# Kernel tuning notes

Hardware: AMD Instinct MI355X
Metric: run time of the kernel (lower is better)

## Reference

```python
import jax, jax.numpy as jnp
import numpy as np

C = 1.0          # Poincare ball curvature
EPS = 1e-7       # clamp epsilon used by the torch code


def _expmap0(u, c=C):
    # geoopt PoincareBall.expmap0: tanh(sqrt(c)||u||) * u / (sqrt(c)||u||)
    sc = jnp.sqrt(c)
    n = jnp.maximum(jnp.linalg.norm(u, axis=-1, keepdims=True), 1e-15)
    return jnp.tanh(sc * n) * u / (sc * n)


def _hyp_dist_sq(x, y, c=C):
    # Pairwise squared Poincare distance WITHOUT materializing [nq,nc,d]:
    # d(x,y) = (2/sqrt(c)) * artanh(sqrt(c) * ||mobius_add(-x, y)||)
    # ||mobius_add(-x,y)||^2 expands into dot products and squared norms.
    dot = x @ y.T                                  # [nq, nc]
    xn = jnp.sum(x * x, axis=-1)[:, None]          # [nq, 1]
    yn = jnp.sum(y * y, axis=-1)[None, :]          # [1, nc]
    alpha = 1.0 - 2.0 * c * dot + c * yn
    beta = 1.0 - c * xn
    num_sq = alpha * alpha * xn - 2.0 * alpha * beta * dot + beta * beta * yn
    den = jnp.maximum(1.0 - 2.0 * c * dot + c * c * xn * yn, 1e-15)
    t = jnp.sqrt(c) * jnp.sqrt(jnp.maximum(num_sq, 0.0)) / den
    t = jnp.clip(t, 0.0, 1.0 - EPS)
    d = (2.0 / jnp.sqrt(c)) * jnp.arctanh(t)
    return d * d


def _project(x, We, be, Wh, bh, Ws, bs, scale_h):
    e = x @ We.T + be
    e = e / jnp.linalg.norm(e, axis=-1, keepdims=True)
    h = _expmap0((x @ Wh.T + bh) * scale_h)
    s = x @ Ws.T + bs
    s = s / jnp.linalg.norm(s, axis=-1, keepdims=True)
    return e, h, s


def setup_inputs() -> dict:
    key = jax.random.key(0)
    ks = jax.random.split(key, 12)
    D, NQ, NC = 768, 512, 65536
    def lin(k, out_d, in_d):
        lim = 1.0 / np.sqrt(in_d)
        k1, k2 = jax.random.split(k)
        W = jax.random.uniform(k1, (out_d, in_d), jnp.float32, -lim, lim)
        b = jax.random.uniform(k2, (out_d,), jnp.float32, -lim, lim)
        return W, b
    We, be = lin(ks[0], 32, D)
    Wh, bh = lin(ks[1], 16, D)
    Ws, bs = lin(ks[2], 16, D)
    W1, b1 = lin(ks[3], 32, D)
    W2, b2 = lin(ks[4], 3, 32)
    return {
        'x_q': jax.random.normal(ks[5], (NQ, D), jnp.float32),
        'x_c': jax.random.normal(ks[6], (NC, D), jnp.float32),
        'We': We, 'be': be, 'Wh': Wh, 'bh': bh, 'Ws': Ws, 'bs': bs,
        'scale_h': jnp.float32(0.3),
        'W1': W1, 'b1': b1, 'W2': W2, 'b2': b2,
    }


def reference(x_q, x_c, We, be, Wh, bh, Ws, bs, scale_h, W1, b1, W2, b2):
    # forward() projections for queries and corpus
    q_e, q_h, q_s = _project(x_q, We, be, Wh, bh, Ws, bs, scale_h)
    c_e, c_h, c_s = _project(x_c, We, be, Wh, bh, Ws, bs, scale_h)
    # get_weights(): softplus MLP on raw query embedding -> [nq, 3]
    w = jax.nn.softplus(jax.nn.relu(x_q @ W1.T + b1) @ W2.T + b2)
    # batch_retrieve math, fully vectorized
    dist_e = 2.0 - 2.0 * (q_e @ c_e.T)                       # unit vecs: ||a-b||^2
    dots = jnp.clip(q_s @ c_s.T, -1.0 + EPS, 1.0 - EPS)
    dist_s = jnp.arccos(dots) ** 2
    dist_h = _hyp_dist_sq(q_h, c_h)
    total = w[:, 0:1] * dist_e + w[:, 1:2] * dist_h + w[:, 2:3] * dist_s
    return -total
```

## Files before the change

kernel.cpp:

```cpp
#include <hip/hip_runtime.h>
#include <math.h>

#define NQ 512
#define NC 65536
#define DIM 768
#define PC_ROWS 128

typedef unsigned short u16;
typedef float f32x4 __attribute__((ext_vector_type(4)));
typedef short bf16x8 __attribute__((ext_vector_type(8)));

#define MFMA16(A, B, C) __builtin_amdgcn_mfma_f32_16x16x32_bf16(A, B, C, 0, 0, 0)

__device__ __forceinline__ u16 f2bf(float x) {
  union { float f; unsigned int u; } v; v.f = x;
  unsigned int r = v.u + 0x7fffu + ((v.u >> 16) & 1u);
  return (u16)(r >> 16);
}
__device__ __forceinline__ float bf2f(u16 h) {
  union { unsigned int u; float f; } v; v.u = ((unsigned int)h) << 16;
  return v.f;
}
__device__ __forceinline__ unsigned int pk2(u16 a, u16 b) {
  return (unsigned int)a | ((unsigned int)b << 16);
}

__device__ __forceinline__ float acos_poly(float x) {
  float z = fabsf(x);
  float p = -0.0012624911f;
  p = fmaf(p, z, 0.0066700901f);
  p = fmaf(p, z, -0.0170881256f);
  p = fmaf(p, z, 0.0308918810f);
  p = fmaf(p, z, -0.0501743046f);
  p = fmaf(p, z, 0.0889789874f);
  p = fmaf(p, z, -0.2145988016f);
  p = fmaf(p, z, 1.5707963050f);
  float r = __builtin_amdgcn_sqrtf(1.0f - z) * p;
  return (x < 0.0f) ? (3.14159265358979f - r) : r;
}

__global__ __launch_bounds__(256) void build_wpak(
    const float* __restrict__ We, const float* __restrict__ Ws,
    const float* __restrict__ Wh, u16* __restrict__ wpak)
{
  int id = blockIdx.x * 256 + threadIdx.x;
  int j = id & 7;
  int lane = (id >> 3) & 63;
  int nt = (id >> 9) & 3;
  int kc = id >> 11;
  int o = nt * 16 + (lane & 15);
  int k = kc * 32 + ((lane >> 4) & 3) * 8 + j;
  const float* Wrow = (o < 32) ? We + (size_t)o * DIM
                    : (o < 48) ? Ws + (size_t)(o - 32) * DIM
                               : Wh + (size_t)(o - 48) * DIM;
  float w = Wrow[k];
  u16 hi = f2bf(w);
  u16 lo = f2bf(w - bf2f(hi));
  size_t base = (((size_t)kc * 4 + nt) * 2 * 64 + lane) * 8 + j;
  wpak[base] = hi;
  wpak[base + 512] = lo;
}

__global__ __launch_bounds__(128) void proj_q(
    const float* __restrict__ xq,
    const float* __restrict__ We, const float* __restrict__ be,
    const float* __restrict__ Wh, const float* __restrict__ bh,
    const float* __restrict__ Ws, const float* __restrict__ bs,
    const float* __restrict__ shp,
    const float* __restrict__ W1, const float* __restrict__ b1,
    const float* __restrict__ W2, const float* __restrict__ b2,
    u16* __restrict__ qpak, float* __restrict__ qmeta)
{
  __shared__ __align__(16) float xrow[DIM];
  __shared__ float vals[96];
  __shared__ float reluv[32];
  __shared__ float hv[16];
  __shared__ float stats[8];
  const int t = threadIdx.x;
  const int q = blockIdx.x;

  for (int i = t; i < DIM; i += 128) xrow[i] = xq[(size_t)q * DIM + i];
  __syncthreads();

  if (t < 96) {
    const float* wr;
    float bias;
    if (t < 32)      { wr = We + (size_t)t * DIM;        bias = be[t]; }
    else if (t < 48) { wr = Ws + (size_t)(t - 32) * DIM; bias = bs[t - 32]; }
    else if (t < 64) { wr = Wh + (size_t)(t - 48) * DIM; bias = bh[t - 48]; }
    else             { wr = W1 + (size_t)(t - 64) * DIM; bias = b1[t - 64]; }
    const float4* x4 = (const float4*)xrow;
    const float4* w4 = (const float4*)wr;
    float acc = 0.0f;
    #pragma unroll 4
    for (int k = 0; k < DIM / 4; ++k) {
      float4 a = x4[k];
      float4 b = w4[k];
      acc = fmaf(a.x, b.x, acc);
      acc = fmaf(a.y, b.y, acc);
      acc = fmaf(a.z, b.z, acc);
      acc = fmaf(a.w, b.w, acc);
    }
    acc += bias;
    if (t >= 48 && t < 64) acc *= shp[0];
    vals[t] = acc;
  }
  __syncthreads();
  if (t < 32) reluv[t] = fmaxf(vals[64 + t], 0.0f);
  __syncthreads();

  if (t == 0) {
    float s = 0.0f;
    for (int j = 0; j < 32; ++j) s += vals[j] * vals[j];
    stats[0] = sqrtf(s);
  } else if (t == 1) {
    float s = 0.0f;
    for (int j = 32; j < 48; ++j) s += vals[j] * vals[j];
    stats[1] = sqrtf(s);
  } else if (t == 2) {
    float s = 0.0f;
    for (int j = 48; j < 64; ++j) s += vals[j] * vals[j];
    float n = fmaxf(sqrtf(s), 1e-15f);
    float f = tanhf(n) / n;
    float xn = 0.0f;
    for (int j = 0; j < 16; ++j) {
      float hj = vals[48 + j] * f;
      hv[j] = hj;
      xn += hj * hj;
    }
    stats[2] = xn;
    stats[3] = 1.0f - xn;
  } else if (t >= 3 && t < 6) {
    int m = t - 3;
    float s = 0.0f;
    for (int j = 0; j < 32; ++j) s = fmaf(reluv[j], W2[m * 32 + j], s);
    s += b2[m];
    stats[4 + m] = fmaxf(s, 0.0f) + log1pf(expf(-fabsf(s)));
  }
  __syncthreads();

  u16* qp = qpak + (size_t)q * 192;
  if (t < 32) {
    float v = vals[t] / stats[0];
    u16 hi = f2bf(v);
    u16 lo = f2bf(v - bf2f(hi));
    qp[t] = hi; qp[32 + t] = lo;
  } else if (t < 48) {
    int j = t - 32;
    float v = vals[t] / stats[1];
    u16 hi = f2bf(v);
    u16 lo = f2bf(v - bf2f(hi));
    qp[64 + j] = hi;  qp[80 + j] = hi;
    qp[96 + j] = lo;  qp[112 + j] = lo;
  } else if (t < 64) {
    int j = t - 48;
    float v = hv[j];
    u16 hi = f2bf(v);
    u16 lo = f2bf(v - bf2f(hi));
    qp[128 + j] = hi; qp[144 + j] = hi;
    qp[160 + j] = lo; qp[176 + j] = lo;
  } else if (t == 64) qmeta[(size_t)q * 8 + 0] = stats[2];
  else if (t == 65)   qmeta[(size_t)q * 8 + 1] = stats[3];
  else if (t >= 66 && t < 69) qmeta[(size_t)q * 8 + (t - 66 + 2)] = stats[4 + (t - 66)];
}

__global__ __launch_bounds__(256) void proj_corpus(
    const float* __restrict__ xc, const u16* __restrict__ wpak,
    const float* __restrict__ be, const float* __restrict__ bh,
    const float* __restrict__ bs, const float* __restrict__ shp,
    u16* __restrict__ cpak, float* __restrict__ cyn)
{
  __shared__ float lds[8320];
  u16* xpk = (u16*)lds;
  float (*vals)[65] = (float(*)[65])lds;
  __shared__ float biasc[64];
  __shared__ float shv;

  const int tid = threadIdx.x;
  const int lane = tid & 63;
  const int wv = tid >> 6;
  const int lr = lane & 15;
  const int lg = lane >> 4;
  const int r0 = blockIdx.x * PC_ROWS;

  if (tid < 64) {
    biasc[tid] = (tid < 32) ? be[tid] : (tid < 48) ? bs[tid - 32] : bh[tid - 48];
    if (tid == 0) shv = shp[0];
  }

  f32x4 acc[2][4];
  #pragma unroll
  for (int rt = 0; rt < 2; ++rt)
    #pragma unroll
    for (int nt = 0; nt < 4; ++nt)
      acc[rt][nt] = (f32x4){0.0f, 0.0f, 0.0f, 0.0f};

  for (int kc = 0; kc < 24; ++kc) {
    __syncthreads();
    #pragma unroll
    for (int i = 0; i < 4; ++i) {
      int p = tid + 256 * i;
      int row = p >> 3;
      int kq = p & 7;
      const float4 v = *(const float4*)(xc + (size_t)(r0 + row) * DIM + kc * 32 + 4 * kq);
      u16 hx = f2bf(v.x), hy = f2bf(v.y), hz = f2bf(v.z), hw = f2bf(v.w);
      u16 lx = f2bf(v.x - bf2f(hx)), ly = f2bf(v.y - bf2f(hy));
      u16 lz = f2bf(v.z - bf2f(hz)), lw = f2bf(v.w - bf2f(hw));
      uint2 hvv = {pk2(hx, hy), pk2(hz, hw)};
      uint2 lvv = {pk2(lx, ly), pk2(lz, lw)};
      int rm = row & 7;
      int qh = (kq >> 1) ^ rm;
      int ql = (4 + (kq >> 1)) ^ rm;
      int half = (kq & 1) * 8;
      *(uint2*)((char*)xpk + row * 128 + qh * 16 + half) = hvv;
      *(uint2*)((char*)xpk + row * 128 + ql * 16 + half) = lvv;
    }
    __syncthreads();

    const u16* wb = wpak + (size_t)kc * 4096;
    bf16x8 Bh[4], Bl[4];
    #pragma unroll
    for (int nt = 0; nt < 4; ++nt) {
      Bh[nt] = *(const bf16x8*)(wb + (nt * 2 + 0) * 512 + lane * 8);
      Bl[nt] = *(const bf16x8*)(wb + (nt * 2 + 1) * 512 + lane * 8);
    }

    #pragma unroll
    for (int rt = 0; rt < 2; ++rt) {
      int rowi = wv * 32 + rt * 16 + lr;
      int rm = rowi & 7;
      bf16x8 Ah = *(const bf16x8*)((const char*)xpk + rowi * 128 + (lg ^ rm) * 16);
      bf16x8 Al = *(const bf16x8*)((const char*)xpk + rowi * 128 + ((4 + lg) ^ rm) * 16);
      #pragma unroll
      for (int nt = 0; nt < 4; ++nt) {
        acc[rt][nt] = MFMA16(Ah, Bh[nt], acc[rt][nt]);
        acc[rt][nt] = MFMA16(Al, Bh[nt], acc[rt][nt]);
        acc[rt][nt] = MFMA16(Ah, Bl[nt], acc[rt][nt]);
      }
    }
  }
  __syncthreads();

  #pragma unroll
  for (int rt = 0; rt < 2; ++rt)
    #pragma unroll
    for (int nt = 0; nt < 4; ++nt)
      #pragma unroll
      for (int reg = 0; reg < 4; ++reg) {
        int row = wv * 32 + rt * 16 + lg * 4 + reg;
        int o = nt * 16 + lr;
        float v = acc[rt][nt][reg] + biasc[o];
        if (o >= 48) v *= shv;
        vals[row][o] = v;
      }
  __syncthreads();

  const int part = tid >> 7;
  const int row = tid & 127;
  const size_t g = (size_t)(r0 + row);
  u16* cp = cpak + g * 128;
  if (part == 0) {
    float ssum = 0.0f;
    for (int j = 0; j < 32; ++j) ssum += vals[row][j] * vals[row][j];
    float inv = 1.0f / sqrtf(ssum);
    for (int j = 0; j < 32; ++j) {
      float v = vals[row][j] * inv;
      u16 hi = f2bf(v);
      cp[j] = hi;
      cp[32 + j] = f2bf(v - bf2f(hi));
    }
  } else {
    float ssum = 0.0f;
    for (int j = 32; j < 48; ++j) ssum += vals[row][j] * vals[row][j];
    float inv = 1.0f / sqrtf(ssum);
    for (int j = 0; j < 16; ++j) {
      float v = vals[row][32 + j] * inv;
      u16 hi = f2bf(v);
      cp[64 + j] = hi;
      cp[80 + j] = f2bf(v - bf2f(hi));
    }
    float hsum = 0.0f;
    for (int j = 48; j < 64; ++j) hsum += vals[row][j] * vals[row][j];
    float n = fmaxf(sqrtf(hsum), 1e-15f);
    float f = tanhf(n) / n;
    float yn = 0.0f;
    for (int j = 0; j < 16; ++j) {
      float hj = vals[row][48 + j] * f;
      u16 hi = f2bf(hj);
      cp[96 + j] = hi;
      cp[112 + j] = f2bf(hj - bf2f(hi));
      yn += hj * hj;
    }
    cyn[g] = yn;
  }
}

#define CLIPC 0.99999988f

__device__ __forceinline__ float pair_score(
    float de, float dss, float dh,
    float xn, float beta, float w0, float w1, float w2, float yn)
{
  float dist_e = 2.0f - 2.0f * de;

  float dcl = fminf(fmaxf(dss, -CLIPC), CLIPC);
  float ac = acos_poly(dcl);
  float dist_s = ac * ac;

  float alpha = 1.0f - 2.0f * dh + yn;
  float ab = alpha * beta;
  float num = alpha * alpha * xn - 2.0f * ab * dh + beta * beta * yn;
  float den = fmaxf(1.0f - 2.0f * dh + xn * yn, 1e-15f);
  float t = __builtin_amdgcn_sqrtf(fmaxf(num, 0.0f)) * __builtin_amdgcn_rcpf(den);
  t = fminf(t, CLIPC);
  float dd = __logf((1.0f + t) * __builtin_amdgcn_rcpf(1.0f - t));
  float dist_h = dd * dd;

  return -(w0 * dist_e + w1 * dist_h + w2 * dist_s);
}

__global__ __launch_bounds__(256) void pairwise(
    const u16* __restrict__ cpak, const float* __restrict__ cyn,
    const u16* __restrict__ qpak, const float* __restrict__ qmeta,
    float* __restrict__ out)
{
  const int lane = threadIdx.x & 63;
  const int wv = threadIdx.x >> 6;
  const int lr = lane & 15;
  const int lg = lane >> 4;
  const int c0 = blockIdx.x * 128 + wv * 32;
  const int qbase = blockIdx.y * 256;

  bf16x8 Beh[2], Bel[2], Bsp[2], Bhp[2];
  float ynv[2];
  #pragma unroll
  for (int ct = 0; ct < 2; ++ct) {
    const u16* cb = cpak + (size_t)(c0 + ct * 16 + lr) * 128 + lg * 8;
    Beh[ct] = *(const bf16x8*)(cb + 0);
    Bel[ct] = *(const bf16x8*)(cb + 32);
    Bsp[ct] = *(const bf16x8*)(cb + 64);
    Bhp[ct] = *(const bf16x8*)(cb + 96);
    ynv[ct] = cyn[c0 + ct * 16 + lr];
  }

  #pragma unroll 1
  for (int qt = 0; qt < 16; ++qt) {
    const int q0 = qbase + qt * 16;
    const u16* qb = qpak + (size_t)(q0 + lr) * 192 + lg * 8;
    bf16x8 Aeh = *(const bf16x8*)(qb + 0);
    bf16x8 Ael = *(const bf16x8*)(qb + 32);
    bf16x8 Ash = *(const bf16x8*)(qb + 64);
    bf16x8 Asl = *(const bf16x8*)(qb + 96);
    bf16x8 Ahh = *(const bf16x8*)(qb + 128);
    bf16x8 Ahl = *(const bf16x8*)(qb + 160);

    float4 mv[4];
    float w2v[4];
    #pragma unroll
    for (int j = 0; j < 4; ++j) {
      const int q = q0 + lg * 4 + j;
      mv[j] = *(const float4*)(qmeta + (size_t)q * 8);
      w2v[j] = qmeta[(size_t)q * 8 + 4];
    }

    const f32x4 z = {0.0f, 0.0f, 0.0f, 0.0f};
    f32x4 aE[2], aS[2], aH[2];
    #pragma unroll
    for (int ct = 0; ct < 2; ++ct) {
      aE[ct] = MFMA16(Aeh, Beh[ct], z);
      aE[ct] = MFMA16(Ael, Beh[ct], aE[ct]);
      aE[ct] = MFMA16(Aeh, Bel[ct], aE[ct]);
      aS[ct] = MFMA16(Ash, Bsp[ct], z);
      aS[ct] = MFMA16(Asl, Bsp[ct], aS[ct]);
      aH[ct] = MFMA16(Ahh, Bhp[ct], z);
      aH[ct] = MFMA16(Ahl, Bhp[ct], aH[ct]);
    }

    #pragma unroll
    for (int j = 0; j < 4; ++j) {
      const int q = q0 + lg * 4 + j;
      #pragma unroll
      for (int ct = 0; ct < 2; ++ct) {
        float r = pair_score(aE[ct][j], aS[ct][j], aH[ct][j],
                             mv[j].x, mv[j].y, mv[j].z, mv[j].w, w2v[j],
                             ynv[ct]);
        out[(size_t)q * NC + c0 + ct * 16 + lr] = r;
      }
    }
  }
}

extern "C" void kernel_launch(void* const* d_in, const int* in_sizes, int n_in,
                              void* d_out, int out_size, void* d_ws, size_t ws_size,
                              hipStream_t stream) {
  const float* xq = (const float*)d_in[0];
  const float* xc = (const float*)d_in[1];
  const float* We = (const float*)d_in[2];
  const float* be = (const float*)d_in[3];
  const float* Wh = (const float*)d_in[4];
  const float* bh = (const float*)d_in[5];
  const float* Ws = (const float*)d_in[6];
  const float* bs = (const float*)d_in[7];
  const float* sh = (const float*)d_in[8];
  const float* W1 = (const float*)d_in[9];
  const float* b1 = (const float*)d_in[10];
  const float* W2 = (const float*)d_in[11];
  const float* b2 = (const float*)d_in[12];
  float* out = (float*)d_out;

  float* w = (float*)d_ws;
  u16* qpak = (u16*)w;
  float* qmeta = w + 49152;
  u16* wpak = (u16*)(qmeta + NQ * 8);
  float* base2 = qmeta + NQ * 8 + 49152;
  u16* cpak = (u16*)base2;
  float* cyn = base2 + 4194304;

  build_wpak<<<192, 256, 0, stream>>>(We, Ws, Wh, wpak);
  proj_q<<<NQ, 128, 0, stream>>>(xq, We, be, Wh, bh, Ws, bs, sh, W1, b1, W2, b2,
                                 qpak, qmeta);
  proj_corpus<<<NC / PC_ROWS, 256, 0, stream>>>(xc, wpak, be, bh, bs, sh, cpak, cyn);
  pairwise<<<dim3(NC / 128, 2, 1), 256, 0, stream>>>(cpak, cyn, qpak, qmeta, out);
}
```

Measured before the change: 445.6 us.

## Prefetch next K-chunk and query tiles into registers; stage query metadata in LDS

In the corpus projection kernel, the global loads of the next 32-column chunk of x_c are issued into registers before the MFMA work of the current chunk, so load latency overlaps compute. In the pairwise kernel, query fragments for the next tile are loaded one iteration ahead (software pipelining), and the per-query metadata is staged once into shared memory instead of being reloaded from global every tile. This raises register pressure, which may lower occupancy, and adds an LDS fill plus a barrier at block start.

```diff
diff --git a/kernel.cpp b/kernel.cpp
--- a/kernel.cpp
+++ b/kernel.cpp
@@ -188,6 +188,15 @@
     if (tid == 0) shv = shp[0];
   }
 
+  const int row0 = tid >> 3,           kq0 = tid & 7;
+  const int row1 = (tid + 256) >> 3,   kq1 = (tid + 256) & 7;
+  const int row2 = (tid + 512) >> 3,   kq2 = (tid + 512) & 7;
+  const int row3 = (tid + 768) >> 3,   kq3 = (tid + 768) & 7;
+  const float* bp0 = xc + (size_t)(r0 + row0) * DIM + 4 * kq0;
+  const float* bp1 = xc + (size_t)(r0 + row1) * DIM + 4 * kq1;
+  const float* bp2 = xc + (size_t)(r0 + row2) * DIM + 4 * kq2;
+  const float* bp3 = xc + (size_t)(r0 + row3) * DIM + 4 * kq3;
+
   f32x4 acc[2][4];
   #pragma unroll
   for (int rt = 0; rt < 2; ++rt)
@@ -195,26 +204,40 @@
     for (int nt = 0; nt < 4; ++nt)
       acc[rt][nt] = (f32x4){0.0f, 0.0f, 0.0f, 0.0f};
 
+  float4 s0 = *(const float4*)(bp0);
+  float4 s1 = *(const float4*)(bp1);
+  float4 s2 = *(const float4*)(bp2);
+  float4 s3 = *(const float4*)(bp3);
+
+  #pragma unroll 1
   for (int kc = 0; kc < 24; ++kc) {
     __syncthreads();
-    #pragma unroll
-    for (int i = 0; i < 4; ++i) {
-      int p = tid + 256 * i;
-      int row = p >> 3;
-      int kq = p & 7;
-      const float4 v = *(const float4*)(xc + (size_t)(r0 + row) * DIM + kc * 32 + 4 * kq);
-      u16 hx = f2bf(v.x), hy = f2bf(v.y), hz = f2bf(v.z), hw = f2bf(v.w);
-      u16 lx = f2bf(v.x - bf2f(hx)), ly = f2bf(v.y - bf2f(hy));
-      u16 lz = f2bf(v.z - bf2f(hz)), lw = f2bf(v.w - bf2f(hw));
-      uint2 hvv = {pk2(hx, hy), pk2(hz, hw)};
-      uint2 lvv = {pk2(lx, ly), pk2(lz, lw)};
-      int rm = row & 7;
-      int qh = (kq >> 1) ^ rm;
-      int ql = (4 + (kq >> 1)) ^ rm;
-      int half = (kq & 1) * 8;
-      *(uint2*)((char*)xpk + row * 128 + qh * 16 + half) = hvv;
-      *(uint2*)((char*)xpk + row * 128 + ql * 16 + half) = lvv;
-    }
+    {
+      const int rows[4] = {row0, row1, row2, row3};
+      const int kqs[4]  = {kq0, kq1, kq2, kq3};
+      float4 sv[4] = {s0, s1, s2, s3};
+      #pragma unroll
+      for (int i = 0; i < 4; ++i) {
+        float4 v = sv[i];
+        u16 hx = f2bf(v.x), hy = f2bf(v.y), hz = f2bf(v.z), hw = f2bf(v.w);
+        u16 lx = f2bf(v.x - bf2f(hx)), ly = f2bf(v.y - bf2f(hy));
+        u16 lz = f2bf(v.z - bf2f(hz)), lw = f2bf(v.w - bf2f(hw));
+        uint2 hvv = {pk2(hx, hy), pk2(hz, hw)};
+        uint2 lvv = {pk2(lx, ly), pk2(lz, lw)};
+        int row = rows[i], kq = kqs[i];
+        int rm = row & 7;
+        int qh = (kq >> 1) ^ rm;
+        int ql = (4 + (kq >> 1)) ^ rm;
+        int half = (kq & 1) * 8;
+        *(uint2*)((char*)xpk + row * 128 + qh * 16 + half) = hvv;
+        *(uint2*)((char*)xpk + row * 128 + ql * 16 + half) = lvv;
+      }
+    }
+    const int kn = (kc < 23) ? (kc + 1) * 32 : kc * 32;
+    s0 = *(const float4*)(bp0 + kn);
+    s1 = *(const float4*)(bp1 + kn);
+    s2 = *(const float4*)(bp2 + kn);
+    s3 = *(const float4*)(bp3 + kn);
     __syncthreads();
 
     const u16* wb = wpak + (size_t)kc * 4096;
@@ -324,8 +347,17 @@
     const u16* __restrict__ qpak, const float* __restrict__ qmeta,
     float* __restrict__ out)
 {
-  const int lane = threadIdx.x & 63;
-  const int wv = threadIdx.x >> 6;
+  __shared__ float4 lmv[NQ];
+  __shared__ float lw2[NQ];
+  const int tid = threadIdx.x;
+  for (int i = tid; i < NQ; i += 256) {
+    const float* m = qmeta + (size_t)i * 8;
+    lmv[i] = *(const float4*)m;
+    lw2[i] = m[4];
+  }
+
+  const int lane = tid & 63;
+  const int wv = tid >> 6;
   const int lr = lane & 15;
   const int lg = lane >> 4;
   const int c0 = blockIdx.x * 128 + wv * 32;
@@ -342,26 +374,28 @@
     Bhp[ct] = *(const bf16x8*)(cb + 96);
     ynv[ct] = cyn[c0 + ct * 16 + lr];
   }
-
-  #pragma unroll 1
+  __syncthreads();
+
+  const u16* qb = qpak + (size_t)(qbase + lr) * 192 + lg * 8;
+  bf16x8 Aeh = *(const bf16x8*)(qb + 0);
+  bf16x8 Ael = *(const bf16x8*)(qb + 32);
+  bf16x8 Ash = *(const bf16x8*)(qb + 64);
+  bf16x8 Asl = *(const bf16x8*)(qb + 96);
+  bf16x8 Ahh = *(const bf16x8*)(qb + 128);
+  bf16x8 Ahl = *(const bf16x8*)(qb + 160);
+
+  #pragma unroll 2
   for (int qt = 0; qt < 16; ++qt) {
     const int q0 = qbase + qt * 16;
-    const u16* qb = qpak + (size_t)(q0 + lr) * 192 + lg * 8;
-    bf16x8 Aeh = *(const bf16x8*)(qb + 0);
-    bf16x8 Ael = *(const bf16x8*)(qb + 32);
-    bf16x8 Ash = *(const bf16x8*)(qb + 64);
-    bf16x8 Asl = *(const bf16x8*)(qb + 96);
-    bf16x8 Ahh = *(const bf16x8*)(qb + 128);
-    bf16x8 Ahl = *(const bf16x8*)(qb + 160);
-
-    float4 mv[4];
-    float w2v[4];
-    #pragma unroll
-    for (int j = 0; j < 4; ++j) {
-      const int q = q0 + lg * 4 + j;
-      mv[j] = *(const float4*)(qmeta + (size_t)q * 8);
-      w2v[j] = qmeta[(size_t)q * 8 + 4];
-    }
+
+    const int qtn = (qt < 15) ? qt + 1 : qt;
+    const u16* qn = qpak + (size_t)(qbase + qtn * 16 + lr) * 192 + lg * 8;
+    bf16x8 Neh = *(const bf16x8*)(qn + 0);
+    bf16x8 Nel = *(const bf16x8*)(qn + 32);
+    bf16x8 Nsh = *(const bf16x8*)(qn + 64);
+    bf16x8 Nsl = *(const bf16x8*)(qn + 96);
+    bf16x8 Nhh = *(const bf16x8*)(qn + 128);
+    bf16x8 Nhl = *(const bf16x8*)(qn + 160);
 
     const f32x4 z = {0.0f, 0.0f, 0.0f, 0.0f};
     f32x4 aE[2], aS[2], aH[2];
@@ -379,14 +413,17 @@
     #pragma unroll
     for (int j = 0; j < 4; ++j) {
       const int q = q0 + lg * 4 + j;
+      const float4 m = lmv[q];
+      const float w2 = lw2[q];
       #pragma unroll
       for (int ct = 0; ct < 2; ++ct) {
         float r = pair_score(aE[ct][j], aS[ct][j], aH[ct][j],
-                             mv[j].x, mv[j].y, mv[j].z, mv[j].w, w2v[j],
-                             ynv[ct]);
+                             m.x, m.y, m.z, m.w, w2, ynv[ct]);
         out[(size_t)q * NC + c0 + ct * 16 + lr] = r;
       }
     }
+
+    Aeh = Neh; Ael = Nel; Ash = Nsh; Asl = Nsl; Ahh = Nhh; Ahl = Nhl;
   }
 }
 
```

Result: no change. 439.4 us (-1.4%).
